# Optimization experiments

Measured on AMD Instinct MI355X. Metric: run time of the kernel, lower is better.

## Reference

```python
import jax, jax.numpy as jnp
import numpy as np
from jax import lax

WINDOW_SIZE = 11
CHANNEL = 3
SIGMA = 1.5
C1 = 0.01 ** 2
C2 = 0.03 ** 2


def _create_window(window_size: int, channel: int) -> jnp.ndarray:
    g = jnp.arange(window_size, dtype=jnp.float32)
    g = jnp.exp(-(g - window_size // 2) ** 2 / (2.0 * SIGMA ** 2))
    g = g / g.sum()
    w2d = g[:, None] * g[None, :]                      # (K, K)
    # HWIO layout for grouped (depthwise) conv: (K, K, 1, channel)
    return jnp.tile(w2d[:, :, None, None], (1, 1, 1, channel))


def _dwconv(x: jnp.ndarray, window: jnp.ndarray) -> jnp.ndarray:
    pad = WINDOW_SIZE // 2
    return lax.conv_general_dilated(
        x, window,
        window_strides=(1, 1),
        padding=((pad, pad), (pad, pad)),
        dimension_numbers=("NCHW", "HWIO", "NCHW"),
        feature_group_count=CHANNEL,
    )


def setup_inputs() -> dict:
    key = jax.random.key(0)
    k1, k2 = jax.random.split(key)
    shape = (16, 3, 512, 512)
    img1 = jax.random.uniform(k1, shape, dtype=jnp.float32)
    img2 = jax.random.uniform(k2, shape, dtype=jnp.float32)
    window = _create_window(WINDOW_SIZE, CHANNEL)
    return {"img1": img1, "img2": img2, "window": window}


def reference(img1, img2, window):
    mu1 = _dwconv(img1, window)
    mu2 = _dwconv(img2, window)
    mu1_sq = mu1 * mu1
    mu2_sq = mu2 * mu2
    mu1_mu2 = mu1 * mu2
    sigma1_sq = _dwconv(img1 * img1, window) - mu1_sq
    sigma2_sq = _dwconv(img2 * img2, window) - mu2_sq
    sigma12 = _dwconv(img1 * img2, window) - mu1_mu2
    ssim_map = ((2.0 * mu1_mu2 + C1) * (2.0 * sigma12 + C2)) / (
        (mu1_sq + mu2_sq + C1) * (sigma1_sq + sigma2_sq + C2)
    )
    return ssim_map.mean()  # size_average=True
```

## Files before the change

kernel.cpp:

```cpp
#include <hip/hip_runtime.h>

#define KW 11
#define PAD 5
#define TW 64
#define TH 32
#define HROWS 16
#define ICOLS 74
#define S4 77
#define SX 77
#define IMH 512
#define IMW 512
#define NBLK 6144
#define NCONV 296
#define LBASE 320
#define NLOAD 192
#define RAWROWS 26
#define RAWV (2*RAWROWS*74)
#define LTASK 21

typedef float f2 __attribute__((ext_vector_type(2)));
typedef float f4 __attribute__((ext_vector_type(4)));


#define A_LOAD(EDGE_)                                                         \
    if (t < NCONV) {                                                          \
        const int gr0 = iy0 + ar0;                                            \
        if (EDGE_) {                                                          \
            const bool cok = (agc >= 0) && (agc < IMW);                       \
            _Pragma("unroll")                                                 \
            for (int i = 0; i < 14; ++i) {                                    \
                const int gr = gr0 + i;                                       \
                const bool ok = cok && (gr >= 0) && (gr < IMH);               \
                const size_t o = base + (size_t)(ok ? gr : 0) * IMW           \
                               + (ok ? agc : 0);                              \
                p1[i] = ok ? img1[o] : 0.f;                                   \
                p2[i] = ok ? img2[o] : 0.f;                                   \
            }                                                                 \
        } else {                                                              \
            _Pragma("unroll")                                                 \
            for (int i = 0; i < 14; ++i) {                                    \
                const size_t o = base + (size_t)(gr0 + i) * IMW + agc;        \
                p1[i] = img1[o];                                              \
                p2[i] = img2[o];                                              \
            }                                                                 \
        }                                                                     \
    }

#define RAW_STAGE(EDGE_)                                                      \
    {                                                                         \
        float rv[LTASK];                                                      \
        _Pragma("unroll")                                                     \
        for (int s = 0; s < LTASK; ++s) {                                     \
            const int o = lidx + NLOAD * s;                                   \
            const int row = o / 148;                                          \
            const int col = (o % 148) >> 1;                                   \
            const int gr = iy1 + row;            \
            const int gc = ix0 + col;                                         \
            const float* sp = (o & 1) ? img2 : img1;                          \
            bool ok = (s != LTASK - 1) || (o < RAWV);                         \
            if (EDGE_) ok = ok && (gr < IMH) && (gc >= 0) && (gc < IMW);      \
            const size_t go = base + (size_t)(ok ? gr : 0) * IMW              \
                            + (ok ? gc : 0);                                  \
            rv[s] = ok ? sp[go] : 0.f;                                        \
        }                                                                     \
        _Pragma("unroll")                                                     \
        for (int s = 0; s < LTASK; ++s) {                                     \
            const int o = lidx + NLOAD * s;                                   \
            if (s != LTASK - 1 || o < RAWV) raw[o] = rv[s];                   \
        }                                                                     \
    }

#define A_CONV_BODY(GETX_)                                                    \
    {                                                                         \
        f2 m12[4]  = {{0,0},{0,0},{0,0},{0,0}};                               \
        f2 qq[4]   = {{0,0},{0,0},{0,0},{0,0}};                               \
        f2 sx01 = {0, 0}, sx23 = {0, 0};                                      \
        _Pragma("unroll")                                                     \
        for (int i = 0; i < 14; ++i) {                                        \
            f2 x12; GETX_;                                                    \
            const f2 sq = x12 * x12;                                          \
            const float sxy = x12.x * x12.y;                                  \
            f2 sxy2; sxy2.x = sxy; sxy2.y = sxy;                              \
            _Pragma("unroll")                                                 \
            for (int k = 0; k < 4; ++k) {                                     \
                const int j = i - k;                                          \
                if (j >= 0 && j < KW) {                                       \
                    const float w = wg[j];                  \
                    const f2 w2 = {w, w};                                     \
                    m12[k] += w2 * x12;                     \
                    qq[k]  += w2 * sq;                      \
                }                                                             \
            }                                                                 \
            if (i >= 1 && i <= 10)       sx01 += wp[i] * sxy2;                \
            else if (i == 0)             sx01.x += wg[0]  * sxy;              \
            else if (i == 11)            sx01.y += wg[10] * sxy;              \
            if (i >= 3 && i <= 12)       sx23 += wp[i - 2] * sxy2;            \
            else if (i == 2)             sx23.x += wg[0]  * sxy;              \
            else if (i == 13)            sx23.y += wg[10] * sxy;              \
        }                                                                     \
        const float sxs[4] = {sx01.x, sx01.y, sx23.x, sx23.y};                \
        _Pragma("unroll")                                                     \
        for (int k = 0; k < 4; ++k) {                                         \
            f4 v;                                                             \
            v.x = m12[k].x; v.y = m12[k].y;                                   \
            v.z = qq[k].x;  v.w = qq[k].y;                                    \
            vv4[(ar0 + k) * S4 + ac] = v;                  \
            vsx[(ar0 + k) * SX + ac] = sxs[k];             \
        }                                                                     \
    }

#define PHASE_B(H_)                                                           \
    {                                                                         \
        const int row = t & 15;                                               \
        const int cp  = t >> 4;                                    \
        const f4* __restrict__ p4 = &vv4[row * S4 + cp * 2];                  \
        const float* __restrict__ px = &vsx[row * SX + cp * 2];               \
        f2 am12[2] = {{0,0},{0,0}};                                           \
        f2 aqq[2]  = {{0,0},{0,0}};                                           \
        f2 asxp = {0, 0};                                                     \
        _Pragma("unroll")                                                     \
        for (int b = 0; b < 3; ++b) {                                         \
            f4 v[4]; float vx[4];                                             \
            _Pragma("unroll")                                                 \
            for (int cc = 0; cc < 4; ++cc) {                                  \
                v[cc]  = p4[b * 4 + cc];                                      \
                vx[cc] = px[b * 4 + cc];                                      \
            }                                                                 \
            _Pragma("unroll")                                                 \
            for (int cc = 0; cc < 4; ++cc) {                                  \
                const int cg = b * 4 + cc;                                    \
                f2 v12; v12.x = v[cc].x; v12.y = v[cc].y;                     \
                f2 vqq; vqq.x = v[cc].z; vqq.y = v[cc].w;                     \
                _Pragma("unroll")                                             \
                for (int k = 0; k < 2; ++k) {                                 \
                    const int j = cg - k;                                     \
                    if (j >= 0 && j < KW) {                                   \
                        const float w = wg[j];                                \
                        const f2 w2 = {w, w};                                 \
                        am12[k] += w2 * v12;                                  \
                        aqq[k]  += w2 * vqq;                                  \
                    }                                                         \
                }                                                             \
                f2 vx2; vx2.x = vx[cc]; vx2.y = vx[cc];                       \
                if (cg >= 1 && cg <= 10)  asxp += wp[cg] * vx2;               \
                else if (cg == 0)         asxp.x += wg[0]  * vx[cc];          \
                else if (cg == 11)        asxp.y += wg[10] * vx[cc];          \
            }                                                                 \
        }                                                                     \
        const float asx[2] = {asxp.x, asxp.y};                                \
        _Pragma("unroll")                                                     \
        for (int k = 0; k < 2; ++k) {                                         \
            const float mu1 = am12[k].x, mu2 = am12[k].y;                     \
            const float mu1sq = mu1 * mu1, mu2sq = mu2 * mu2;                 \
            const float mu12 = mu1 * mu2;                                     \
            const float sig1 = aqq[k].x - mu1sq;                              \
            const float sig2 = aqq[k].y - mu2sq;                              \
            const float sig12 = asx[k] - mu12;                                \
            const float num = (2.f * mu12 + C1v) * (2.f * sig12 + C2v);       \
            const float den = (mu1sq + mu2sq + C1v) * (sig1 + sig2 + C2v);    \
            float r = __builtin_amdgcn_rcpf(den);                             \
            r = r * (2.f - den * r);               \
            lsum += num * r;                                                  \
        }                                                                     \
    }

__global__ __launch_bounds__(512, 4) void ssim_main(
    const float* __restrict__ img1, const float* __restrict__ img2,
    const float* __restrict__ window, float* __restrict__ partial)
{
    __shared__ f4 vv4[HROWS * S4];
    __shared__ float vsx[HROWS * SX];
    __shared__ __align__(16) float raw[RAWV];
    __shared__ float g[KW];
    __shared__ float wsum[8];

    const int t = threadIdx.x;

    const int plane = blockIdx.z;
    const size_t base = (size_t)plane * IMH * IMW;
    const int ix0 = blockIdx.x * TW - PAD;
    const int iy0 = blockIdx.y * TH - PAD;
    const int iy1 = iy0 + HROWS;

    const int ac  = t % ICOLS;
    const int ar0 = (t / ICOLS) * 4;
    const int agc = ix0 + ac;
    const int lidx = t - LBASE;

    const bool interior = (ix0 >= 0) && (ix0 + ICOLS <= IMW) &&
                          (iy0 >= 0) && (iy0 + TH + KW - 1 <= IMH);

    float p1[14], p2[14];

    if (t < LBASE) {
        if (interior) { A_LOAD(false) } else { A_LOAD(true) }
    } else {
        if (interior) { RAW_STAGE(false) } else { RAW_STAGE(true) }
    }

    if (t < KW) {
        float s = 0.f;
        for (int j = 0; j < KW; ++j) s += window[(t * KW + j) * 3];
        g[t] = s;
    }
    __syncthreads();

    float wg[KW];
#pragma unroll
    for (int j = 0; j < KW; ++j) {
        const int bi = __builtin_amdgcn_readfirstlane(__float_as_int(g[j]));
        wg[j] = __int_as_float(bi);
    }
    f2 wp[KW];
#pragma unroll
    for (int j = 1; j < KW; ++j) { wp[j].x = wg[j]; wp[j].y = wg[j - 1]; }

    const float C1v = 0.0001f;
    const float C2v = 0.0009f;
    float lsum = 0.f;

    if (t < NCONV) A_CONV_BODY(x12.x = p1[i]; x12.y = p2[i];)
    __syncthreads();

    PHASE_B(0)
    __syncthreads();

    if (t < NCONV)
        A_CONV_BODY(x12 = *reinterpret_cast<const f2*>(
                        &raw[((ar0 + i) * 74 + ac) * 2]);)
    __syncthreads();

    PHASE_B(1)

#pragma unroll
    for (int off = 32; off > 0; off >>= 1) lsum += __shfl_down(lsum, off, 64);
    if ((t & 63) == 0) wsum[t >> 6] = lsum;
    __syncthreads();
    if (t == 0) {
        float bs = 0.f;
#pragma unroll
        for (int w = 0; w < 8; ++w) bs += wsum[w];
        unsigned bid = (blockIdx.z * gridDim.y + blockIdx.y) * gridDim.x
                     + blockIdx.x;
        partial[bid] = bs;
    }
}

__global__ __launch_bounds__(1024) void ssim_reduce(
    const float* __restrict__ partial, float* __restrict__ out, double inv_n)
{
    __shared__ double dsum[16];
    const int t = threadIdx.x;
    double s = 0.0;
    for (int i = t; i < NBLK; i += 1024) s += (double)partial[i];
#pragma unroll
    for (int off = 32; off > 0; off >>= 1) s += __shfl_down(s, off, 64);
    if ((t & 63) == 0) dsum[t >> 6] = s;
    __syncthreads();
    if (t == 0) {
        double tot = 0.0;
#pragma unroll
        for (int w = 0; w < 16; ++w) tot += dsum[w];
        out[0] = (float)(tot * inv_n);
    }
}

extern "C" void kernel_launch(void* const* d_in, const int* in_sizes, int n_in,
                              void* d_out, int out_size, void* d_ws, size_t ws_size,
                              hipStream_t stream) {
    const float* img1   = (const float*)d_in[0];
    const float* img2   = (const float*)d_in[1];
    const float* window = (const float*)d_in[2];
    float* out = (float*)d_out;
    float* partial = (float*)d_ws;

    const int nplanes = in_sizes[0] / (IMH * IMW);
    const long long total = (long long)in_sizes[0];

    dim3 grid(IMW / TW, IMH / TH, nplanes);
    ssim_main<<<grid, 512, 0, stream>>>(img1, img2, window, partial);
    ssim_reduce<<<1, 1024, 0, stream>>>(partial, out, 1.0 / (double)total);
}
```

Before: 159.0 us.

## Process four row strips per block with prefetched raw loads overlapping compute

Each block now covers 64 output rows as four 16-row strips instead of two, halving the block count. Global loads for the next strip are issued into registers during the current strip's vertical pass and written to shared memory after a barrier, overlapping memory latency with compute. The taller tile cuts the redundant halo-row loads per output. In exchange the kernel holds more live registers, has more barriers per block, and launches fewer blocks, which may reduce occupancy and parallelism.

```diff
diff --git a/kernel.cpp b/kernel.cpp
--- a/kernel.cpp
+++ b/kernel.cpp
@@ -3,14 +3,15 @@
 #define KW 11
 #define PAD 5
 #define TW 64
-#define TH 32
+#define TH 64
 #define HROWS 16
+#define NSTRIP 4
 #define ICOLS 74
 #define S4 77
 #define SX 77
 #define IMH 512
 #define IMW 512
-#define NBLK 6144
+#define NBLK 3072
 #define NCONV 296
 #define LBASE 320
 #define NLOAD 192
@@ -46,15 +47,15 @@
         }                                                                     \
     }
 
-#define RAW_STAGE(EDGE_)                                                      \
+#define RAW_ISSUE(EDGE_, S_)                                                  \
     {                                                                         \
-        float rv[LTASK];                                                      \
+        const int iyS = iy0 + (S_) * HROWS;                                   \
         _Pragma("unroll")                                                     \
         for (int s = 0; s < LTASK; ++s) {                                     \
             const int o = lidx + NLOAD * s;                                   \
             const int row = o / 148;                                          \
             const int col = (o % 148) >> 1;                                   \
-            const int gr = iy1 + row;            \
+            const int gr = iyS + row;                                         \
             const int gc = ix0 + col;                                         \
             const float* sp = (o & 1) ? img2 : img1;                          \
             bool ok = (s != LTASK - 1) || (o < RAWV);                         \
@@ -63,6 +64,10 @@
                             + (ok ? gc : 0);                                  \
             rv[s] = ok ? sp[go] : 0.f;                                        \
         }                                                                     \
+    }
+
+#define RAW_WRITE                                                             \
+    {                                                                         \
         _Pragma("unroll")                                                     \
         for (int s = 0; s < LTASK; ++s) {                                     \
             const int o = lidx + NLOAD * s;                                   \
@@ -109,7 +114,7 @@
         }                                                                     \
     }
 
-#define PHASE_B(H_)                                                           \
+#define PHASE_B                                                               \
     {                                                                         \
         const int row = t & 15;                                               \
         const int cp  = t >> 4;                                    \
@@ -180,7 +185,6 @@
     const size_t base = (size_t)plane * IMH * IMW;
     const int ix0 = blockIdx.x * TW - PAD;
     const int iy0 = blockIdx.y * TH - PAD;
-    const int iy1 = iy0 + HROWS;
 
     const int ac  = t % ICOLS;
     const int ar0 = (t / ICOLS) * 4;
@@ -191,11 +195,13 @@
                           (iy0 >= 0) && (iy0 + TH + KW - 1 <= IMH);
 
     float p1[14], p2[14];
+    float rv[LTASK];
 
     if (t < LBASE) {
         if (interior) { A_LOAD(false) } else { A_LOAD(true) }
     } else {
-        if (interior) { RAW_STAGE(false) } else { RAW_STAGE(true) }
+        if (interior) { RAW_ISSUE(false, 1) } else { RAW_ISSUE(true, 1) }
+        RAW_WRITE
     }
 
     if (t < KW) {
@@ -220,17 +226,37 @@
     float lsum = 0.f;
 
     if (t < NCONV) A_CONV_BODY(x12.x = p1[i]; x12.y = p2[i];)
-    __syncthreads();
-
-    PHASE_B(0)
+    else if (t >= LBASE) {
+        if (interior) { RAW_ISSUE(false, 2) } else { RAW_ISSUE(true, 2) }
+    }
+    __syncthreads();
+    PHASE_B
     __syncthreads();
 
     if (t < NCONV)
         A_CONV_BODY(x12 = *reinterpret_cast<const f2*>(
                         &raw[((ar0 + i) * 74 + ac) * 2]);)
     __syncthreads();
-
-    PHASE_B(1)
+    if (t >= LBASE) RAW_WRITE
+    PHASE_B
+    __syncthreads();
+
+    if (t < NCONV)
+        A_CONV_BODY(x12 = *reinterpret_cast<const f2*>(
+                        &raw[((ar0 + i) * 74 + ac) * 2]);)
+    else if (t >= LBASE) {
+        if (interior) { RAW_ISSUE(false, 3) } else { RAW_ISSUE(true, 3) }
+    }
+    __syncthreads();
+    if (t >= LBASE) RAW_WRITE
+    PHASE_B
+    __syncthreads();
+
+    if (t < NCONV)
+        A_CONV_BODY(x12 = *reinterpret_cast<const f2*>(
+                        &raw[((ar0 + i) * 74 + ac) * 2]);)
+    __syncthreads();
+    PHASE_B
 
 #pragma unroll
     for (int off = 32; off > 0; off >>= 1) lsum += __shfl_down(lsum, off, 64);
```

Result: slower. 178.8 us (+12.4%).
